# Optimization experiments

Hardware: AMD Instinct MI355X
Metric: run time of the kernel (lower is better)

Reference implementation:

```python
import jax, jax.numpy as jnp
import numpy as np

B, D_IN, D_HID, D_OUT = 16384, 512, 512, 512
E, K = 8, 2
VQ_COEFF, LB_COEFF = 0.05, 0.01
LOG100 = float(np.log(100.0))
LOG2 = float(np.log(2.0))


def _normalize(v):
    # torch F.normalize(dim=1): x / max(||x||, 1e-12)
    n = jnp.linalg.norm(v, axis=-1, keepdims=True)
    return v / jnp.maximum(n, 1e-12)


def _cv_squared(v):
    # torch .var() is unbiased (ddof=1)
    return jnp.var(v, ddof=1) / (jnp.mean(v) ** 2 + 1e-10)


def _rbm_layer(x, rm, W, b, ca, temp):
    # x: [B, d_in], rm: [E, d_in], W: [E, d_out, d_in], b: [E, d_out]
    rm_n = jax.lax.stop_gradient(_normalize(rm))          # .detach() in source
    nx = _normalize(x)
    dists = nx @ rm_n.T                                    # [B, E]
    top_v, top_i = jax.lax.top_k(dists, K)                 # [B, K]
    tv = jax.nn.softmax(top_v, axis=-1)                    # softmax over top-k
    bsz = dists.shape[0]
    attn = jnp.zeros_like(dists).at[jnp.arange(bsz)[:, None], top_i].set(tv)
    # const_attention is frozen (requires_grad=False)
    inp_att = jnp.exp(jnp.minimum(jax.lax.stop_gradient(ca), LOG100))  # [E]
    # dense gather-compute-scatter: expert e output for every token, masked by attn
    eo = jnp.einsum('bi,eoi->beo', x, W) * inp_att[None, :, None] + b[None, :, :]
    out = jnp.einsum('be,beo->bo', jax.lax.stop_gradient(attn), eo)    # att.detach()
    out = out * jnp.exp(jnp.minimum(temp, LOG100))
    # aux losses (eval mode: no EMA memory update)
    vq = -(nx[:, None, :] * rm_n[top_i]).sum(-1)           # [B, K]
    vq_loss = (tv * vq).sum(-1).mean()
    lb = _cv_squared(attn.sum(0))
    aux = VQ_COEFF * vq_loss + LB_COEFF * lb               # sim_coeff = 0
    return out, aux


def setup_inputs() -> dict:
    key = jax.random.key(0)
    ks = jax.random.split(key, 8)
    x = jax.random.normal(ks[0], (B, D_IN), dtype=jnp.float32)
    rm0 = _normalize(jax.random.normal(ks[1], (E, D_IN), dtype=jnp.float32))
    W0 = jax.random.normal(ks[2], (E, D_HID, D_IN), dtype=jnp.float32) / np.sqrt(D_IN)
    b0 = jnp.zeros((E, D_HID), dtype=jnp.float32)
    rm1 = _normalize(jax.random.normal(ks[3], (E, D_HID), dtype=jnp.float32))
    W1 = jax.random.normal(ks[4], (E, D_OUT, D_HID), dtype=jnp.float32) / np.sqrt(D_HID)
    b1 = jnp.zeros((E, D_OUT), dtype=jnp.float32)
    temp0 = jnp.full((1,), LOG2, dtype=jnp.float32)
    temp1 = jnp.full((1,), LOG2, dtype=jnp.float32)
    ca0 = jnp.zeros((E,), dtype=jnp.float32)
    ca1 = jnp.zeros((E,), dtype=jnp.float32)
    return {"x": x, "rm0": rm0, "W0": W0, "b0": b0, "temp0": temp0, "ca0": ca0,
            "rm1": rm1, "W1": W1, "b1": b1, "temp1": temp1, "ca1": ca1}


def reference(x, rm0, W0, b0, temp0, ca0, rm1, W1, b1, temp1, ca1):
    h0, a0 = _rbm_layer(x, rm0, W0, b0, ca0, temp0)
    h_emb = h0                      # embedding tapped after layer 0 (pre-activation)
    h = jax.nn.relu(h0)             # norm_type=None -> no norm
    h1, a1 = _rbm_layer(h, rm1, W1, b1, ca1, temp1)
    return (h_emb, h1, a0 + a1)
```

## Files before the change

kernel.cpp:

```cpp
#include <hip/hip_runtime.h>
#include <cmath>
#include <cstdint>

#define NTOK   16384
#define DM     512
#define NEXP   8
#define LOG100 4.605170185988092f

typedef _Float16 half8  __attribute__((ext_vector_type(8)));
typedef _Float16 half4  __attribute__((ext_vector_type(4)));
typedef float    floatx4 __attribute__((ext_vector_type(4)));

#define MFMA_F16(a, b, c) __builtin_amdgcn_mfma_f32_16x16x32_f16((a), (b), (c), 0, 0, 0)

__device__ __forceinline__ void gl_lds16(const void* g, void* l) {
    __builtin_amdgcn_global_load_lds(
        (const __attribute__((address_space(1))) void*)g,
        (__attribute__((address_space(3))) void*)l, 16, 0, 0);
}


__global__ __launch_bounds__(256) void prep_kernel(
    const float* __restrict__ rm0, const float* __restrict__ rm1,
    const float* __restrict__ ca0, const float* __restrict__ ca1,
    const float* __restrict__ temp0, const float* __restrict__ temp1,
    float* __restrict__ ctrl, float* __restrict__ rmn)
{
    int tid = threadIdx.x, lane = tid & 63, w = tid >> 6;
    if (tid < 32) ((int*)ctrl)[tid] = 0;
    if (tid >= 32 && tid < 48) ctrl[tid] = 0.f;
    if (tid == 48 || tid == 49) ctrl[tid] = 0.f;
    if (tid == 50) ctrl[50] = expf(fminf(temp0[0], LOG100));
    if (tid == 51) ctrl[51] = expf(fminf(temp1[0], LOG100));
    if (tid >= 52 && tid < 68) {
        int i = tid - 52;
        ctrl[tid] = expf(fminf(i < 8 ? ca0[i] : ca1[i - 8], LOG100));
    }
    for (int r = w; r < 16; r += 4) {
        const float* src = (r < 8) ? (rm0 + r * DM) : (rm1 + (r - 8) * DM);
        float v[8]; float ss = 0.f;
        #pragma unroll
        for (int j = 0; j < 8; ++j) { v[j] = src[lane + 64 * j]; ss += v[j] * v[j]; }
        #pragma unroll
        for (int off = 32; off > 0; off >>= 1) ss += __shfl_xor(ss, off);
        float inv = 1.f / fmaxf(sqrtf(ss), 1e-12f);
        float* dst = rmn + r * DM;
        #pragma unroll
        for (int j = 0; j < 8; ++j) dst[lane + 64 * j] = v[j] * inv;
    }
}

__global__ __launch_bounds__(256) void conv_w_kernel(
    const float4* __restrict__ W0, const float4* __restrict__ W1,
    half4* __restrict__ w0hi, half4* __restrict__ w0lo, half4* __restrict__ w1h)
{
    int i = blockIdx.x * 256 + threadIdx.x;
    float4 a = W0[i], b = W1[i];
    const float* ap = (const float*)&a;
    const float* bp = (const float*)&b;
    half4 hi, lo, h1;
    #pragma unroll
    for (int j = 0; j < 4; ++j) {
        _Float16 h = (_Float16)ap[j];
        hi[j] = h;
        lo[j] = (_Float16)(ap[j] - (float)h);
        h1[j] = (_Float16)bp[j];
    }
    w0hi[i] = hi; w0lo[i] = lo; w1h[i] = h1;
}

__global__ __launch_bounds__(256) void route_kernel(
    const float* __restrict__ src,
    const float* __restrict__ rmn,
    int relu_in,
    _Float16* __restrict__ dst_hi,
    _Float16* __restrict__ dst_lo,
    unsigned char* __restrict__ key,
    float2* __restrict__ wts,
    float2* __restrict__ bs)
{
    __shared__ float rmLds[NEXP * DM];
    int tid = threadIdx.x;
    for (int i = tid; i < NEXP * DM; i += 256) rmLds[i] = rmn[i];
    __syncthreads();
    int lane = tid & 63, w = tid >> 6;
    int token = blockIdx.x * 4 + w;

    const float* row = src + (size_t)token * DM;
    float x[8]; float ss = 0.f;
    #pragma unroll
    for (int j = 0; j < 8; ++j) {
        float v = row[lane + 64 * j];
        if (relu_in) v = fmaxf(v, 0.f);
        x[j] = v; ss += v * v;
    }
    #pragma unroll
    for (int j = 0; j < 8; ++j) {
        _Float16 h = (_Float16)x[j];
        dst_hi[(size_t)token * DM + lane + 64 * j] = h;
        if (dst_lo) dst_lo[(size_t)token * DM + lane + 64 * j] = (_Float16)(x[j] - (float)h);
    }
    float d[8];
    #pragma unroll
    for (int e = 0; e < 8; ++e) {
        float a = 0.f;
        #pragma unroll
        for (int j = 0; j < 8; ++j) a += x[j] * rmLds[e * DM + lane + 64 * j];
        d[e] = a;
    }
    #pragma unroll
    for (int off = 32; off > 0; off >>= 1) {
        ss += __shfl_xor(ss, off);
        #pragma unroll
        for (int e = 0; e < 8; ++e) d[e] += __shfl_xor(d[e], off);
    }
    float inv = 1.f / fmaxf(sqrtf(ss), 1e-12f);
    float best = -1e30f, second = -1e30f; int be = 0, se = 0;
    #pragma unroll
    for (int e = 0; e < 8; ++e) {
        float de = d[e] * inv;
        if (de > best)        { second = best; se = be; best = de; be = e; }
        else if (de > second) { second = de; se = e; }
    }
    float z = expf(second - best);
    float w0 = 1.f / (1.f + z), w1 = z / (1.f + z);
    if (lane == 0) {
        key[token] = (unsigned char)be;
        key[NTOK + token] = (unsigned char)se;
        wts[token] = make_float2(w0, w1);
        bs[token] = make_float2(best, second);
    }
}

__global__ __launch_bounds__(256) void compact_kernel(
    const unsigned char* __restrict__ key,
    const float2* __restrict__ wts,
    const float2* __restrict__ bs,
    int* __restrict__ cnt,
    unsigned short* __restrict__ bkt,
    float* __restrict__ imp,
    float* __restrict__ vq_acc)
{
    int slot = blockIdx.x >> 3, e = blockIdx.x & 7;
    const unsigned char* k = key + slot * NTOK;
    unsigned short* ob = bkt + (size_t)(slot * 8 + e) * NTOK;
    __shared__ int wc[2][4];
    int tid = threadIdx.x, lane = tid & 63, w = tid >> 6;
    int base = 0;
    float wsum = 0.f, vqs = 0.f;
    for (int c = 0; c < 64; ++c) {
        int tok = c * 256 + tid;
        bool m = (k[tok] == (unsigned char)e);
        unsigned long long mask = __ballot(m);
        int p = c & 1;
        if (lane == 0) wc[p][w] = __popcll(mask);
        __syncthreads();
        int off = base;
        for (int i = 0; i < w; ++i) off += wc[p][i];
        if (m) {
            int pre = __popcll(mask & ((1ull << lane) - 1ull));
            ob[off + pre] = (unsigned short)tok;
            float2 wp = wts[tok]; float2 b2 = bs[tok];
            float wv = slot ? wp.y : wp.x;
            wsum += wv;
            vqs  += wv * (slot ? b2.y : b2.x);
        }
        base += wc[p][0] + wc[p][1] + wc[p][2] + wc[p][3];
    }
    #pragma unroll
    for (int off = 32; off > 0; off >>= 1) {
        wsum += __shfl_xor(wsum, off);
        vqs  += __shfl_xor(vqs, off);
    }
    __shared__ float rw[4], rv[4];
    if (lane == 0) { rw[w] = wsum; rv[w] = vqs; }
    __syncthreads();
    if (tid == 0) {
        cnt[slot * 8 + e] = base;
        float W = rw[0] + rw[1] + rw[2] + rw[3];
        float V = rv[0] + rv[1] + rv[2] + rv[3];
        atomicAdd(&imp[e], W);
        atomicAdd(vq_acc, -V);
    }
}

template <bool SPLIT>
__global__ __launch_bounds__(256) void gemm_kernel(
    const _Float16* __restrict__ Ahi, const _Float16* __restrict__ Alo,
    const _Float16* __restrict__ Whi, const _Float16* __restrict__ Wlo,
    const float* __restrict__ bias,
    const float* __restrict__ iav,
    const float* __restrict__ tscp,
    const int* __restrict__ cnt,
    const unsigned short* __restrict__ bkt,
    const float2* __restrict__ wts,
    int slot, int accum,
    float* __restrict__ outp)
{
    __shared__ __align__(16) _Float16 lds[2 * 128 * 64];
    __shared__ int tokLds[128];
    _Float16* tA = lds;
    _Float16* tB = lds + 128 * 64;

    int e = blockIdx.x >> 7, mt = blockIdx.x & 127;
    int M = cnt[e];
    int m0 = mt << 7;
    if (m0 >= M) return;
    int n0 = blockIdx.y << 7;
    int valid = min(128, M - m0);
    int tid = threadIdx.x, lane = tid & 63, w = tid >> 6;
    if (tid < 128) tokLds[tid] = bkt[e * NTOK + m0 + min(tid, valid - 1)];
    __syncthreads();

    floatx4 acc[4][4];
    #pragma unroll
    for (int mi = 0; mi < 4; ++mi)
        #pragma unroll
        for (int ni = 0; ni < 4; ++ni) acc[mi][ni] = (floatx4){0.f, 0.f, 0.f, 0.f};

    const _Float16* WbH = Whi + ((size_t)e * DM + n0) * DM;
    const _Float16* WbL = SPLIT ? (Wlo + ((size_t)e * DM + n0) * DM) : nullptr;

    int subRow = lane >> 3, p = lane & 7;
    int cSt = p ^ (subRow & 7);
    int wm = w >> 1, wn = w & 1;
    int r0 = wm * 64, c0 = wn * 64;
    int q = lane >> 4, l15 = lane & 15;

    constexpr int KIT = SPLIT ? 16 : 8;
    constexpr int KSTEP = SPLIT ? 32 : 64;

    for (int kb = 0; kb < KIT; ++kb) {
        int k0 = kb * KSTEP;
        #pragma unroll
        for (int j = w; j < 16; j += 4) {
            int row = j * 8 + subRow;
            int tok = tokLds[row];
            const _Float16* g;
            if constexpr (SPLIT)
                g = (cSt < 4) ? (Ahi + (size_t)tok * DM + k0 + cSt * 8)
                              : (Alo + (size_t)tok * DM + k0 + (cSt - 4) * 8);
            else
                g = Ahi + (size_t)tok * DM + k0 + cSt * 8;
            gl_lds16(g, (void*)(tA + j * 512));
        }
        #pragma unroll
        for (int j = w; j < 16; j += 4) {
            int row = j * 8 + subRow;
            const _Float16* g;
            if constexpr (SPLIT)
                g = (cSt < 4) ? (WbH + (size_t)row * DM + k0 + cSt * 8)
                              : (WbL + (size_t)row * DM + k0 + (cSt - 4) * 8);
            else
                g = WbH + (size_t)row * DM + k0 + cSt * 8;
            gl_lds16(g, (void*)(tB + j * 512));
        }
        __syncthreads();

        if constexpr (SPLIT) {
            half8 ah[4], al[4];
            #pragma unroll
            for (int mi = 0; mi < 4; ++mi) {
                int r = r0 + mi * 16 + l15;
                int ph = q ^ (r & 7), pl = (q + 4) ^ (r & 7);
                ah[mi] = *(const half8*)(tA + r * 64 + ph * 8);
                al[mi] = *(const half8*)(tA + r * 64 + pl * 8);
            }
            #pragma unroll
            for (int ni = 0; ni < 4; ++ni) {
                int r = c0 + ni * 16 + l15;
                int ph = q ^ (r & 7), pl = (q + 4) ^ (r & 7);
                half8 bh = *(const half8*)(tB + r * 64 + ph * 8);
                half8 bl = *(const half8*)(tB + r * 64 + pl * 8);
                #pragma unroll
                for (int mi = 0; mi < 4; ++mi) acc[mi][ni] = MFMA_F16(ah[mi], bh, acc[mi][ni]);
                #pragma unroll
                for (int mi = 0; mi < 4; ++mi) acc[mi][ni] = MFMA_F16(ah[mi], bl, acc[mi][ni]);
                #pragma unroll
                for (int mi = 0; mi < 4; ++mi) acc[mi][ni] = MFMA_F16(al[mi], bh, acc[mi][ni]);
            }
        } else {
            #pragma unroll
            for (int ks = 0; ks < 2; ++ks) {
                half8 a[4];
                #pragma unroll
                for (int mi = 0; mi < 4; ++mi) {
                    int r = r0 + mi * 16 + l15;
                    int pc = (ks * 4 + q) ^ (r & 7);
                    a[mi] = *(const half8*)(tA + r * 64 + pc * 8);
                }
                #pragma unroll
                for (int ni = 0; ni < 4; ++ni) {
                    int r = c0 + ni * 16 + l15;
                    int pc = (ks * 4 + q) ^ (r & 7);
                    half8 b = *(const half8*)(tB + r * 64 + pc * 8);
                    #pragma unroll
                    for (int mi = 0; mi < 4; ++mi) acc[mi][ni] = MFMA_F16(a[mi], b, acc[mi][ni]);
                }
            }
        }
        __syncthreads();
    }

    float t = *tscp, iae = iav[e];
    float bv[4];
    #pragma unroll
    for (int ni = 0; ni < 4; ++ni) bv[ni] = bias[e * DM + n0 + c0 + ni * 16 + l15];
    #pragma unroll
    for (int mi = 0; mi < 4; ++mi) {
        int liBase = r0 + mi * 16 + q * 4;
        #pragma unroll
        for (int reg = 0; reg < 4; ++reg) {
            int li = liBase + reg;
            if (li < valid) {
                int tok = tokLds[li];
                float2 wp = wts[tok];
                float wgt = slot ? wp.y : wp.x;
                float sg = t * wgt * iae, sb = t * wgt;
                float* orow = outp + (size_t)tok * DM + n0;
                #pragma unroll
                for (int ni = 0; ni < 4; ++ni) {
                    float v = acc[mi][ni][reg] * sg + bv[ni] * sb;
                    int c = c0 + ni * 16 + l15;
                    if (accum) orow[c] += v; else orow[c] = v;
                }
            }
        }
    }
}

__global__ void finalize_kernel(const float* __restrict__ ctrl, float* __restrict__ outp)
{
    if (threadIdx.x == 0) {
        float aux = 0.f;
        for (int l = 0; l < 2; ++l) {
            float vq = ctrl[48 + l] / (float)NTOK;
            float mean = 0.f;
            for (int e = 0; e < 8; ++e) mean += ctrl[32 + l * 8 + e];
            mean *= 0.125f;
            float s = 0.f;
            for (int e = 0; e < 8; ++e) {
                float d = ctrl[32 + l * 8 + e] - mean;
                s += d * d;
            }
            float var = s / 7.f;
            float lb = var / (mean * mean + 1e-10f);
            aux += 0.05f * vq + 0.01f * lb;
        }
        *outp = aux;
    }
}

extern "C" void kernel_launch(void* const* d_in, const int* in_sizes, int n_in,
                              void* d_out, int out_size, void* d_ws, size_t ws_size,
                              hipStream_t stream) {
    const float* x     = (const float*)d_in[0];
    const float* rm0   = (const float*)d_in[1];
    const float* W0    = (const float*)d_in[2];
    const float* b0    = (const float*)d_in[3];
    const float* temp0 = (const float*)d_in[4];
    const float* ca0   = (const float*)d_in[5];
    const float* rm1   = (const float*)d_in[6];
    const float* W1    = (const float*)d_in[7];
    const float* b1    = (const float*)d_in[8];
    const float* temp1 = (const float*)d_in[9];
    const float* ca1   = (const float*)d_in[10];
    float* out = (float*)d_out;

    char* ws = (char*)d_ws;
    float* ctrl = (float*)ws;
    int*   cnt  = (int*)ctrl;
    float* imp  = ctrl + 32;
    float* vq   = ctrl + 48;
    float* tsc  = ctrl + 50;
    float* ia   = ctrl + 52;
    float* rmn  = ctrl + 128;
    float2*        wts = (float2*)(ws + (size_t)64  * 1024);
    float2*        bs  = (float2*)(ws + (size_t)384 * 1024);
    unsigned char* key = (unsigned char*)(ws + (size_t)704 * 1024);

    char* big = ws + (1 << 20);
    half4*          w0hi4 = (half4*)(big);
    half4*          w0lo4 = (half4*)(big + (size_t)4  * 1024 * 1024);
    half4*          w1h4  = (half4*)(big + (size_t)8  * 1024 * 1024);
    _Float16*       w0hi  = (_Float16*)w0hi4;
    _Float16*       w0lo  = (_Float16*)w0lo4;
    _Float16*       w1h   = (_Float16*)w1h4;
    _Float16*       h16   = (_Float16*)(big + (size_t)12 * 1024 * 1024);
    unsigned short* bkt   = (unsigned short*)(big + (size_t)28 * 1024 * 1024);

    _Float16* xhi = (_Float16*)(out + (size_t)NTOK * DM);
    _Float16* xlo = xhi + (size_t)NTOK * DM;

    prep_kernel<<<1, 256, 0, stream>>>(rm0, rm1, ca0, ca1, temp0, temp1, ctrl, rmn);
    conv_w_kernel<<<2048, 256, 0, stream>>>((const float4*)W0, (const float4*)W1,
                                            w0hi4, w0lo4, w1h4);

    route_kernel<<<4096, 256, 0, stream>>>(x, rmn, 0, xhi, xlo,
        key, wts, bs);
    compact_kernel<<<16, 256, 0, stream>>>(key, wts, bs, cnt, bkt, imp, vq);
    gemm_kernel<true><<<dim3(1024, 4), 256, 0, stream>>>(xhi, xlo, w0hi, w0lo, b0, ia, tsc,
        cnt, bkt, wts, 0, 0, out);
    gemm_kernel<true><<<dim3(1024, 4), 256, 0, stream>>>(xhi, xlo, w0hi, w0lo, b0, ia, tsc,
        cnt + 8, bkt + 8 * NTOK, wts, 1, 1, out);

    route_kernel<<<4096, 256, 0, stream>>>(out, rmn + 4096, 1, h16, (_Float16*)nullptr,
        key + 2 * NTOK, wts + NTOK, bs + NTOK);
    compact_kernel<<<16, 256, 0, stream>>>(key + 2 * NTOK, wts + NTOK, bs + NTOK,
        cnt + 16, bkt + 16 * NTOK, imp + 8, vq + 1);
    gemm_kernel<false><<<dim3(1024, 4), 256, 0, stream>>>(h16, (const _Float16*)nullptr, w1h,
        (const _Float16*)nullptr, b1, ia + 8, tsc + 1,
        cnt + 16, bkt + 16 * NTOK, wts + NTOK, 0, 0, out + (size_t)NTOK * DM);
    gemm_kernel<false><<<dim3(1024, 4), 256, 0, stream>>>(h16, (const _Float16*)nullptr, w1h,
        (const _Float16*)nullptr, b1, ia + 8, tsc + 1,
        cnt + 24, bkt + 24 * NTOK, wts + NTOK, 1, 1, out + (size_t)NTOK * DM);

    finalize_kernel<<<1, 64, 0, stream>>>(ctrl, out + (size_t)2 * NTOK * DM);
}
```

Baseline: 492.6 us.

## Merge both top-k slot GEMMs into one launch using atomic accumulation

Each layer's two per-slot expert GEMM launches become a single launch with a flattened 1D grid over expert, N-tile, slot and M-tile. Results are combined with unsafe atomic adds into an output buffer that the routing kernel now zero-fills ahead of time. The intent is to remove one launch and its serialization and tail per layer, with both slots' work running concurrently. The GEMM inner loop also precomputes global and LDS pointers once instead of recomputing swizzled addresses every k-step. The cost is fp32 atomic traffic on the output plus an extra zero-store pass, and the floating-point summation order is no longer deterministic.

```diff
diff --git a/kernel.cpp b/kernel.cpp
--- a/kernel.cpp
+++ b/kernel.cpp
@@ -75,6 +75,7 @@
     int relu_in,
     _Float16* __restrict__ dst_hi,
     _Float16* __restrict__ dst_lo,
+    float* __restrict__ zbase,
     unsigned char* __restrict__ key,
     float2* __restrict__ wts,
     float2* __restrict__ bs)
@@ -99,6 +100,12 @@
         _Float16 h = (_Float16)x[j];
         dst_hi[(size_t)token * DM + lane + 64 * j] = h;
         if (dst_lo) dst_lo[(size_t)token * DM + lane + 64 * j] = (_Float16)(x[j] - (float)h);
+    }
+    {
+        float4 z = make_float4(0.f, 0.f, 0.f, 0.f);
+        float4* zr = (float4*)(zbase + (size_t)token * DM);
+        zr[lane * 2] = z;
+        zr[lane * 2 + 1] = z;
     }
     float d[8];
     #pragma unroll
@@ -194,7 +201,6 @@
     const int* __restrict__ cnt,
     const unsigned short* __restrict__ bkt,
     const float2* __restrict__ wts,
-    int slot, int accum,
     float* __restrict__ outp)
 {
     __shared__ __align__(16) _Float16 lds[2 * 128 * 64];
@@ -202,14 +208,17 @@
     _Float16* tA = lds;
     _Float16* tB = lds + 128 * 64;
 
-    int e = blockIdx.x >> 7, mt = blockIdx.x & 127;
-    int M = cnt[e];
+    int bx = blockIdx.x;
+    int e = bx & 7; int r = bx >> 3;
+    int n0 = (r & 3) << 7; r >>= 2;
+    int slot = r & 1; int mt = r >> 1;
+    int M = cnt[slot * 8 + e];
     int m0 = mt << 7;
     if (m0 >= M) return;
-    int n0 = blockIdx.y << 7;
     int valid = min(128, M - m0);
     int tid = threadIdx.x, lane = tid & 63, w = tid >> 6;
-    if (tid < 128) tokLds[tid] = bkt[e * NTOK + m0 + min(tid, valid - 1)];
+    const unsigned short* ob = bkt + (size_t)(slot * 8 + e) * NTOK;
+    if (tid < 128) tokLds[tid] = ob[m0 + min(tid, valid - 1)];
     __syncthreads();
 
     floatx4 acc[4][4];
@@ -230,48 +239,64 @@
     constexpr int KIT = SPLIT ? 16 : 8;
     constexpr int KSTEP = SPLIT ? 32 : 64;
 
+    const _Float16* aPtr[4]; const _Float16* bPtr[4];
+    _Float16* aDst[4]; _Float16* bDst[4];
+    #pragma unroll
+    for (int jj = 0; jj < 4; ++jj) {
+        int j = w + jj * 4;
+        int row = j * 8 + subRow;
+        int tok = tokLds[row];
+        if constexpr (SPLIT) {
+            aPtr[jj] = (cSt < 4) ? (Ahi + (size_t)tok * DM + cSt * 8)
+                                 : (Alo + (size_t)tok * DM + (cSt - 4) * 8);
+            bPtr[jj] = (cSt < 4) ? (WbH + (size_t)row * DM + cSt * 8)
+                                 : (WbL + (size_t)row * DM + (cSt - 4) * 8);
+        } else {
+            aPtr[jj] = Ahi + (size_t)tok * DM + cSt * 8;
+            bPtr[jj] = WbH + (size_t)row * DM + cSt * 8;
+        }
+        aDst[jj] = tA + j * 512;
+        bDst[jj] = tB + j * 512;
+    }
+    const half8 *aHp[4], *aLp[4], *bHp[4], *bLp[4];
+    #pragma unroll
+    for (int i = 0; i < 4; ++i) {
+        int ra = r0 + i * 16 + l15;
+        int rb = c0 + i * 16 + l15;
+        if constexpr (SPLIT) {
+            aHp[i] = (const half8*)(tA + ra * 64 + ((q) ^ (ra & 7)) * 8);
+            aLp[i] = (const half8*)(tA + ra * 64 + ((q + 4) ^ (ra & 7)) * 8);
+            bHp[i] = (const half8*)(tB + rb * 64 + ((q) ^ (rb & 7)) * 8);
+            bLp[i] = (const half8*)(tB + rb * 64 + ((q + 4) ^ (rb & 7)) * 8);
+        } else {
+            aHp[i] = (const half8*)(tA + ra * 64 + ((q) ^ (ra & 7)) * 8);
+            aLp[i] = (const half8*)(tA + ra * 64 + ((4 + q) ^ (ra & 7)) * 8);
+            bHp[i] = (const half8*)(tB + rb * 64 + ((q) ^ (rb & 7)) * 8);
+            bLp[i] = (const half8*)(tB + rb * 64 + ((4 + q) ^ (rb & 7)) * 8);
+        }
+    }
+
     for (int kb = 0; kb < KIT; ++kb) {
-        int k0 = kb * KSTEP;
-        #pragma unroll
-        for (int j = w; j < 16; j += 4) {
-            int row = j * 8 + subRow;
-            int tok = tokLds[row];
-            const _Float16* g;
-            if constexpr (SPLIT)
-                g = (cSt < 4) ? (Ahi + (size_t)tok * DM + k0 + cSt * 8)
-                              : (Alo + (size_t)tok * DM + k0 + (cSt - 4) * 8);
-            else
-                g = Ahi + (size_t)tok * DM + k0 + cSt * 8;
-            gl_lds16(g, (void*)(tA + j * 512));
-        }
-        #pragma unroll
-        for (int j = w; j < 16; j += 4) {
-            int row = j * 8 + subRow;
-            const _Float16* g;
-            if constexpr (SPLIT)
-                g = (cSt < 4) ? (WbH + (size_t)row * DM + k0 + cSt * 8)
-                              : (WbL + (size_t)row * DM + k0 + (cSt - 4) * 8);
-            else
-                g = WbH + (size_t)row * DM + k0 + cSt * 8;
-            gl_lds16(g, (void*)(tB + j * 512));
+        #pragma unroll
+        for (int jj = 0; jj < 4; ++jj) {
+            gl_lds16(aPtr[jj], (void*)aDst[jj]);
+            aPtr[jj] += KSTEP;
+        }
+        #pragma unroll
+        for (int jj = 0; jj < 4; ++jj) {
+            gl_lds16(bPtr[jj], (void*)bDst[jj]);
+            bPtr[jj] += KSTEP;
         }
         __syncthreads();
 
         if constexpr (SPLIT) {
             half8 ah[4], al[4];
             #pragma unroll
-            for (int mi = 0; mi < 4; ++mi) {
-                int r = r0 + mi * 16 + l15;
-                int ph = q ^ (r & 7), pl = (q + 4) ^ (r & 7);
-                ah[mi] = *(const half8*)(tA + r * 64 + ph * 8);
-                al[mi] = *(const half8*)(tA + r * 64 + pl * 8);
-            }
+            for (int mi = 0; mi < 4; ++mi) { ah[mi] = *aHp[mi]; al[mi] = *aLp[mi]; }
             #pragma unroll
             for (int ni = 0; ni < 4; ++ni) {
-                int r = c0 + ni * 16 + l15;
-                int ph = q ^ (r & 7), pl = (q + 4) ^ (r & 7);
-                half8 bh = *(const half8*)(tB + r * 64 + ph * 8);
-                half8 bl = *(const half8*)(tB + r * 64 + pl * 8);
+                half8 bh = *bHp[ni];
+                half8 bl = *bLp[ni];
                 #pragma unroll
                 for (int mi = 0; mi < 4; ++mi) acc[mi][ni] = MFMA_F16(ah[mi], bh, acc[mi][ni]);
                 #pragma unroll
@@ -280,23 +305,22 @@
                 for (int mi = 0; mi < 4; ++mi) acc[mi][ni] = MFMA_F16(al[mi], bh, acc[mi][ni]);
             }
         } else {
-            #pragma unroll
-            for (int ks = 0; ks < 2; ++ks) {
-                half8 a[4];
-                #pragma unroll
-                for (int mi = 0; mi < 4; ++mi) {
-                    int r = r0 + mi * 16 + l15;
-                    int pc = (ks * 4 + q) ^ (r & 7);
-                    a[mi] = *(const half8*)(tA + r * 64 + pc * 8);
-                }
-                #pragma unroll
-                for (int ni = 0; ni < 4; ++ni) {
-                    int r = c0 + ni * 16 + l15;
-                    int pc = (ks * 4 + q) ^ (r & 7);
-                    half8 b = *(const half8*)(tB + r * 64 + pc * 8);
-                    #pragma unroll
-                    for (int mi = 0; mi < 4; ++mi) acc[mi][ni] = MFMA_F16(a[mi], b, acc[mi][ni]);
-                }
+            half8 a[4];
+            #pragma unroll
+            for (int mi = 0; mi < 4; ++mi) a[mi] = *aHp[mi];
+            #pragma unroll
+            for (int ni = 0; ni < 4; ++ni) {
+                half8 b = *bHp[ni];
+                #pragma unroll
+                for (int mi = 0; mi < 4; ++mi) acc[mi][ni] = MFMA_F16(a[mi], b, acc[mi][ni]);
+            }
+            #pragma unroll
+            for (int mi = 0; mi < 4; ++mi) a[mi] = *aLp[mi];
+            #pragma unroll
+            for (int ni = 0; ni < 4; ++ni) {
+                half8 b = *bLp[ni];
+                #pragma unroll
+                for (int mi = 0; mi < 4; ++mi) acc[mi][ni] = MFMA_F16(a[mi], b, acc[mi][ni]);
             }
         }
         __syncthreads();
@@ -322,7 +346,7 @@
                 for (int ni = 0; ni < 4; ++ni) {
                     float v = acc[mi][ni][reg] * sg + bv[ni] * sb;
                     int c = c0 + ni * 16 + l15;
-                    if (accum) orow[c] += v; else orow[c] = v;
+                    unsafeAtomicAdd(&orow[c], v);
                 }
             }
         }
@@ -391,29 +415,26 @@
 
     _Float16* xhi = (_Float16*)(out + (size_t)NTOK * DM);
     _Float16* xlo = xhi + (size_t)NTOK * DM;
+    float* h0 = out;
+    float* h1 = out + (size_t)NTOK * DM;
 
     prep_kernel<<<1, 256, 0, stream>>>(rm0, rm1, ca0, ca1, temp0, temp1, ctrl, rmn);
     conv_w_kernel<<<2048, 256, 0, stream>>>((const float4*)W0, (const float4*)W1,
                                             w0hi4, w0lo4, w1h4);
 
-    route_kernel<<<4096, 256, 0, stream>>>(x, rmn, 0, xhi, xlo,
+    route_kernel<<<4096, 256, 0, stream>>>(x, rmn, 0, xhi, xlo, h0,
         key, wts, bs);
     compact_kernel<<<16, 256, 0, stream>>>(key, wts, bs, cnt, bkt, imp, vq);
-    gemm_kernel<true><<<dim3(1024, 4), 256, 0, stream>>>(xhi, xlo, w0hi, w0lo, b0, ia, tsc,
-        cnt, bkt, wts, 0, 0, out);
-    gemm_kernel<true><<<dim3(1024, 4), 256, 0, stream>>>(xhi, xlo, w0hi, w0lo, b0, ia, tsc,
-        cnt + 8, bkt + 8 * NTOK, wts, 1, 1, out);
-
-    route_kernel<<<4096, 256, 0, stream>>>(out, rmn + 4096, 1, h16, (_Float16*)nullptr,
+    gemm_kernel<true><<<8192, 256, 0, stream>>>(xhi, xlo, w0hi, w0lo, b0, ia, tsc,
+        cnt, bkt, wts, h0);
+
+    route_kernel<<<4096, 256, 0, stream>>>(h0, rmn + 4096, 1, h16, (_Float16*)nullptr, h1,
         key + 2 * NTOK, wts + NTOK, bs + NTOK);
     compact_kernel<<<16, 256, 0, stream>>>(key + 2 * NTOK, wts + NTOK, bs + NTOK,
         cnt + 16, bkt + 16 * NTOK, imp + 8, vq + 1);
-    gemm_kernel<false><<<dim3(1024, 4), 256, 0, stream>>>(h16, (const _Float16*)nullptr, w1h,
+    gemm_kernel<false><<<8192, 256, 0, stream>>>(h16, (const _Float16*)nullptr, w1h,
         (const _Float16*)nullptr, b1, ia + 8, tsc + 1,
-        cnt + 16, bkt + 16 * NTOK, wts + NTOK, 0, 0, out + (size_t)NTOK * DM);
-    gemm_kernel<false><<<dim3(1024, 4), 256, 0, stream>>>(h16, (const _Float16*)nullptr, w1h,
-        (const _Float16*)nullptr, b1, ia + 8, tsc + 1,
-        cnt + 24, bkt + 24 * NTOK, wts + NTOK, 1, 1, out + (size_t)NTOK * DM);
+        cnt + 16, bkt + 16 * NTOK, wts + NTOK, h1);
 
     finalize_kernel<<<1, 64, 0, stream>>>(ctrl, out + (size_t)2 * NTOK * DM);
 }
```

Result: slower. 509.4 us (+3.4%).
